# Kernel tuning notes

Hardware: AMD Instinct MI355X
Metric: run time of the kernel (lower is better)

Reference implementation:

```python
import jax, jax.numpy as jnp
import numpy as np

B, C_IN, C_OUT, N, T, KT = 8, 32, 64, 512, 24, 3
EPS = 1e-5

def leaky(x):
    return jax.nn.leaky_relu(x, 0.01)

def layer_norm(x, g, b):
    # LayerNorm over last 3 dims [C_OUT, N, T]
    m = x.mean(axis=(1, 2, 3), keepdims=True)
    v = x.var(axis=(1, 2, 3), keepdims=True)
    return (x - m) * jax.lax.rsqrt(v + EPS) * g[None] + b[None]

def conv1d_dil2(x, w):
    # Conv1d(kernel=2, dilation=2, padding=1, no bias); x: (B,C,L), w: (O,C,2)
    return jax.lax.conv_general_dilated(x, w, window_strides=(1,), padding=[(1, 1)],
                                        rhs_dilation=(2,), dimension_numbers=('NCH', 'OIH', 'NCH'))

def setup_inputs():
    key = jax.random.key(0)
    ks = jax.random.split(key, 32)
    x = jax.random.normal(ks[0], (B, C_IN, N, T), jnp.float32)
    mask = jax.random.uniform(ks[1], (N, N)) < 0.02
    adj = jnp.where(mask, jax.random.uniform(ks[2], (N, N)), 0.0).astype(jnp.float32)
    s = 0.05
    p = {
        'conv1_w': jax.random.normal(ks[3], (C_OUT, C_IN)) * s,
        'conv1_b': jnp.zeros((C_OUT,)),
        'tc_w': jax.random.normal(ks[4], (C_OUT, C_IN, 1, KT)) * s,
        'tc_b': jnp.zeros((C_OUT,)),
        'ln_g': jnp.ones((C_OUT, N, T)),
        'ln_b': jnp.zeros((C_OUT, N, T)),
        's0_ws': jax.random.normal(ks[5], (T, T)) * s,
        's0_wn': jax.random.normal(ks[6], (T, T)) * s,
        's0_b': jnp.zeros((T,)),
        's1_ws': jax.random.normal(ks[7], (T, T)) * s,
        's1_wn': jax.random.normal(ks[8], (T, T)) * s,
        's1_b': jnp.zeros((T,)),
        't_w1': jax.random.normal(ks[9], (C_OUT,)) * s,
        't_w2': jax.random.normal(ks[10], (N,)) * s,
        't_wd1': jax.random.normal(ks[11], (T, T, 2)) * s,
        't_wd2': jax.random.normal(ks[12], (C_OUT, C_OUT, 2)) * s,
        't_W': jax.random.normal(ks[13], (N, C_OUT)) * s,
        't_b': jnp.zeros((T, T)),
        't_v': jax.random.normal(ks[14], (T, T)) * s,
        'bn_g': jnp.ones((T,)),
        'bn_b': jnp.zeros((T,)),
    }
    return {'x': x, 'adj': adj, **p}

def _forward(x, adj, conv1_w, conv1_b, tc_w, tc_b, ln_g, ln_b,
             s0_ws, s0_wn, s0_b, s1_ws, s1_wn, s1_b,
             t_w1, t_w2, t_wd1, t_wd2, t_W, t_b, t_v, bn_g, bn_b):
    # 1x1 conv residual branch
    x_input = jnp.einsum('bcnl,oc->bonl', x, conv1_w) + conv1_b[None, :, None, None]
    # temporal conv (1,Kt) padding (0,1)
    x1 = jax.lax.conv_general_dilated(x, tc_w, (1, 1), [(0, 0), (1, 1)],
                                      dimension_numbers=('NCHW', 'OIHW', 'NCHW'))
    x1 = x1 + tc_b[None, :, None, None]
    x1 = leaky(layer_norm(x1, ln_g, ln_b))
    Ls = jnp.stack([jnp.eye(N, dtype=x.dtype) * 4.0, adj])          # (2,N,N)
    h = jnp.einsum('bcnl,knq->bckql', x1, Ls)                        # (B,C_OUT,2,N,T)
    M = (adj != 0).astype(x.dtype)                                   # edges u->v
    deg = jnp.maximum(M.sum(axis=0), 1.0)                            # in-degree per dst
    def sage(h, ws, wn, bias):
        neigh = jnp.einsum('bckul,uv->bckvl', h, M) / deg[None, None, None, :, None]
        return (jnp.einsum('bcknl,ml->bcknm', h, ws)
                + jnp.einsum('bcknl,ml->bcknm', neigh, wn) + bias)
    h = sage(h, s0_ws, s0_wn, s0_b)
    h = sage(h, s1_ws, s1_wn, s1_b)
    x1 = h.reshape(B, 2 * C_OUT, N, T)
    filt, gate = x1[:, :C_OUT], x1[:, C_OUT:]
    x1 = jax.nn.sigmoid(gate) * leaky(filt)                          # (B,C_OUT,N,T)
    # TATT_1
    f1 = jnp.einsum('bcnl,c->bln', x1, t_w1)                         # (B,T,N)
    f1 = conv1d_dil2(f1, t_wd1)                                      # (B,T,N)
    f2 = jnp.einsum('bcnl,n->bcl', x1, t_w2)                         # (B,C_OUT,T)
    f2 = conv1d_dil2(f2, t_wd2)                                      # (B,C_OUT,T)
    logits = jax.nn.sigmoid(jnp.einsum('bln,nc,bcq->blq', f1, t_W, f2) + t_b)
    logits = jnp.einsum('lk,bkq->blq', t_v, logits)                  # (B,T,T)
    # BatchNorm1d(T) on permuted (B,T_q,T_l), training-mode batch stats
    z = logits.transpose(0, 2, 1)
    mu = z.mean(axis=(0, 2), keepdims=True)
    var = z.var(axis=(0, 2), keepdims=True)
    z = (z - mu) * jax.lax.rsqrt(var + EPS) * bn_g[None, :, None] + bn_b[None, :, None]
    logits = z.transpose(0, 2, 1)
    A = np.zeros((T, T), np.float32); A[:12, :12] = 1.0; A[12:, 12:] = 1.0
    Bmask = jnp.asarray(-1e13 * (1.0 - A), jnp.float32)
    coefs = jax.nn.softmax(logits + Bmask, axis=-1)                  # (B,T,T)
    T_coef = coefs.transpose(0, 2, 1)
    x1 = jnp.einsum('bcnl,blq->bcnq', x1, T_coef)
    out = layer_norm(leaky(x1) + x_input, ln_g, ln_b)
    return out, adj, T_coef

def reference(x, adj, conv1_w, conv1_b, tc_w, tc_b, ln_g, ln_b,
              s0_ws, s0_wn, s0_b, s1_ws, s1_wn, s1_b,
              t_w1, t_w2, t_wd1, t_wd2, t_W, t_b, t_v, bn_g, bn_b):
    return _forward(x, adj, conv1_w, conv1_b, tc_w, tc_b, ln_g, ln_b,
                    s0_ws, s0_wn, s0_b, s1_ws, s1_wn, s1_b,
                    t_w1, t_w2, t_wd1, t_wd2, t_W, t_b, t_v, bn_g, bn_b)
```

## Files before the change

### kernel.cpp

```cpp
#include <hip/hip_runtime.h>
#include <hip/hip_bf16.h>
#include <math.h>

#define B_    8
#define CIN   32
#define CO    64
#define NN    512
#define TT    24
#define NT    (NN*TT)
#define LNCNT (CO*NT)
#define EPSL  1e-5f
#define MAXNZ 64
#define HSS   28

typedef const float* fp;
static __device__ __forceinline__ float lk(float x){ return x > 0.f ? x : 0.01f*x; }
static __device__ __forceinline__ float sg(float x){
    if(x >= 0.f){ float e = expf(-x); return 1.f/(1.f+e); }
    float e = expf(x); return e/(1.f+e);
}
static __device__ __forceinline__ unsigned pk2(float a, float b){
    __hip_bfloat16 x = __float2bfloat16(a), y = __float2bfloat16(b);
    unsigned lo = *(unsigned short*)&x, hi = *(unsigned short*)&y;
    return lo | (hi<<16);
}
static __device__ __forceinline__ float lo2f(unsigned u){ return __uint_as_float(u<<16); }
static __device__ __forceinline__ float hi2f(unsigned u){ return __uint_as_float(u & 0xffff0000u); }

__global__ __launch_bounds__(256) void k_csc(fp adj, int* cnt, int* idx, float* val){
    int e = blockIdx.x*blockDim.x + threadIdx.x;
    if(e >= NN*NN) return;
    float a = adj[e];
    if(a != 0.f){
        int u = e >> 9, q = e & 511;
        int slot = atomicAdd(&cnt[q], 1);
        if(slot < MAXNZ){ idx[q*MAXNZ+slot] = u; val[q*MAXNZ+slot] = a; }
    }
}
__global__ void k_deg(int* cnt, float* deginv){
    int q = blockIdx.x*blockDim.x + threadIdx.x;
    if(q < NN){
        int c = cnt[q];
        deginv[q] = 1.f / (c < 1 ? 1.f : (float)c);
        if(c > MAXNZ) cnt[q] = MAXNZ;
    }
}

static __device__ __forceinline__ void ldw_split(fp w, int m, int kb, uint4* hi, uint4* lo){
    float vh[8], vl[8];
    #pragma unroll
    for(int j=0;j<8;++j){
        float v = (m < TT && (kb+j) < TT) ? w[m*TT + kb + j] : 0.f;
        __hip_bfloat16 hb = __float2bfloat16(v);
        float hf = __bfloat162float(hb);
        vh[j] = hf;
        vl[j] = v - hf;
    }
    *hi = make_uint4(pk2(vh[0],vh[1]),pk2(vh[2],vh[3]),pk2(vh[4],vh[5]),pk2(vh[6],vh[7]));
    *lo = make_uint4(pk2(vl[0],vl[1]),pk2(vl[2],vl[3]),pk2(vl[4],vl[5]),pk2(vl[6],vl[7]));
}

__global__ __launch_bounds__(256) void k_wprep(fp s0ws, fp s0wn, fp s1ws, fp s1wn, uint4* wf){
    int t = threadIdx.x;
    int lane = t & 63, g = t >> 6;
    int M = g >> 1, H = g & 1;
    int m  = H*16 + (lane&15);
    int kb = (lane>>4)*8;
    for(int L=0; L<2; ++L){
        fp w = L ? (M ? s1wn : s1ws) : (M ? s0wn : s0ws);
        uint4 hi, lo;
        ldw_split(w, m, kb, &hi, &lo);
        wf[L*512 + g*128 +      lane] = hi;
        wf[L*512 + g*128 + 64 + lane] = lo;
    }
}

__global__ __launch_bounds__(256) void k_wcprep(fp w1, fp wt, uint4* wcf){
    int t = threadIdx.x;
    int lane = t & 63, g = t >> 6;
    int kb = (lane>>4)*8;
    for(int ot=0; ot<4; ++ot){
        int m = ot*16 + (lane&15);
        float vh[8], vl[8];
        #pragma unroll
        for(int j=0;j<8;++j){
            int c = kb+j;
            float v = (g==0) ? w1[m*CIN+c] : wt[(m*CIN+c)*3 + (g-1)];
            __hip_bfloat16 hb = __float2bfloat16(v);
            float hf = __bfloat162float(hb);
            vh[j]=hf; vl[j]=v-hf;
        }
        wcf[ot*512 + g*128 +      lane] = make_uint4(
            pk2(vh[0],vh[1]),pk2(vh[2],vh[3]),pk2(vh[4],vh[5]),pk2(vh[6],vh[7]));
        wcf[ot*512 + g*128 + 64 + lane] = make_uint4(
            pk2(vl[0],vl[1]),pk2(vl[2],vl[3]),pk2(vl[4],vl[5]),pk2(vl[6],vl[7]));
    }
}

typedef __attribute__((ext_vector_type(8))) short bf16x8;
typedef __attribute__((ext_vector_type(4))) float f32x4;

static __device__ __forceinline__ f32x4 MF(uint4 a, uint4 b, f32x4 c){
    union { uint4 u; bf16x8 v; } A, Bv; A.u = a; Bv.u = b;
    return __builtin_amdgcn_mfma_f32_16x16x32_bf16(A.v, Bv.v, c, 0, 0, 0);
}

#define XST 20
__global__ __launch_bounds__(256, 4) void k_conv(fp x, const uint4* wcf, fp b1, fp bt,
        float* xin, float* x1p, float* stats){
    __shared__ __attribute__((aligned(16))) unsigned xh[208*XST];
    __shared__ __attribute__((aligned(16))) unsigned xl[208*XST];
    __shared__ float red[256];
    int bid = blockIdx.x; int b = bid>>6; int n0 = (bid&63)*8;
    int tid = threadIdx.x; int lane = tid&63; int w = tid>>6;
    for(int i=tid;i<3072;i+=256){
        int cp = i/192; int r = i-cp*192; int node = r/24; int t = r-node*24;
        const float* xp = x + ((size_t)(b*CIN + 2*cp)*NN + n0+node)*TT + t;
        float a = xp[0], b2 = xp[NT];
        __hip_bfloat16 ab = __float2bfloat16(a), bb = __float2bfloat16(b2);
        float ah = __bfloat162float(ab), bh = __bfloat162float(bb);
        int row = node*26 + t + 1;
        xh[row*XST+cp] = pk2(ah, bh);
        xl[row*XST+cp] = pk2(a-ah, b2-bh);
    }
    {
        int node = tid>>5; int which = (tid>>4)&1; int j = tid&15;
        int row = node*26 + which*25;
        xh[row*XST+j]=0; xl[row*XST+j]=0;
    }
    const uint4* wb = wcf + w*512;
    uint4 h1 = wb[      lane], l1 = wb[ 64+lane];
    uint4 ht0= wb[128 + lane], lt0= wb[192+lane];
    uint4 ht1= wb[256 + lane], lt1= wb[320+lane];
    uint4 ht2= wb[384 + lane], lt2= wb[448+lane];
    int mrow = (lane>>4)*4;
    float bi0[4], bi1[4];
    #pragma unroll
    for(int r2=0;r2<4;++r2){
        int o = w*16 + mrow + r2;
        bi0[r2]=b1[o]; bi1[r2]=bt[o];
    }
    __syncthreads();
    float ls=0.f, lsq=0.f;
    int kb4 = (lane>>4)*4;
    for(int pt=0; pt<12; ++pt){
        int p = pt*16 + (lane&15);
        int node = p/24, t = p-node*24;
        int rc = (node*26 + t + 1)*XST;
        uint4 Bhm = *(const uint4*)&xh[rc - XST + kb4];
        uint4 Blm = *(const uint4*)&xl[rc - XST + kb4];
        uint4 Bhc = *(const uint4*)&xh[rc       + kb4];
        uint4 Blc = *(const uint4*)&xl[rc       + kb4];
        uint4 Bhp = *(const uint4*)&xh[rc + XST + kb4];
        uint4 Blp = *(const uint4*)&xl[rc + XST + kb4];
        f32x4 D0 = {bi0[0],bi0[1],bi0[2],bi0[3]};
        f32x4 D1 = {bi1[0],bi1[1],bi1[2],bi1[3]};
        D0 = MF(h1, Bhc, D0); D0 = MF(l1, Bhc, D0); D0 = MF(h1, Blc, D0);
        D1 = MF(ht0,Bhm, D1); D1 = MF(lt0,Bhm, D1); D1 = MF(ht0,Blm, D1);
        D1 = MF(ht1,Bhc, D1); D1 = MF(lt1,Bhc, D1); D1 = MF(ht1,Blc, D1);
        D1 = MF(ht2,Bhp, D1); D1 = MF(lt2,Bhp, D1); D1 = MF(ht2,Blp, D1);
        size_t gbase = ((size_t)(b*CO + w*16 + mrow)*NN + n0+node)*TT + t;
        #pragma unroll
        for(int r2=0;r2<4;++r2){
            xin[gbase + (size_t)r2*NT] = D0[r2];
            x1p[gbase + (size_t)r2*NT] = D1[r2];
            ls  += D1[r2];
            lsq += D1[r2]*D1[r2];
        }
    }
    red[tid]=ls; __syncthreads();
    for(int s=128;s>0;s>>=1){ if(tid<s) red[tid]+=red[tid+s]; __syncthreads(); }
    float tsum = red[0]; __syncthreads();
    red[tid]=lsq; __syncthreads();
    for(int s=128;s>0;s>>=1){ if(tid<s) red[tid]+=red[tid+s]; __syncthreads(); }
    if(tid==0){ atomicAdd(&stats[b], tsum); atomicAdd(&stats[8+b], red[0]); }
}

__global__ void k_stat(float* stats, int off){
    int b = threadIdx.x;
    if(b < 8){
        float m = stats[off+b] / (float)LNCNT;
        float v = stats[off+8+b] / (float)LNCNT - m*m;
        v = fmaxf(v, 0.f);
        stats[off+16+b] = m;
        stats[off+24+b] = rsqrtf(v + EPSL);
    }
}

__global__ __launch_bounds__(256) void k_hbuild(fp x1p, fp lng, fp lnb,
        const float* stats, const int* cnt, const int* idx, const float* val, unsigned* h){
    __shared__ float xs[NN*HSS];
    int blk = blockIdx.x; int b = blk >> 6; int c = blk & 63;
    int tid = threadIdx.x;
    float m = stats[16+b], inv = stats[24+b];
    fp src = x1p + (size_t)(b*CO + c)*NT;
    for(int i=tid;i<NT;i+=256){
        int n = i/TT, t = i%TT;
        xs[n*HSS + t] = lk((src[i] - m)*inv*lng[c*NT + i] + lnb[c*NT + i]);
    }
    __syncthreads();
    unsigned* h0 = h + (size_t)((b*CO+c)*2 + 0)*(NT/2);
    unsigned* h1 = h0 + NT/2;
    #pragma unroll
    for(int half=0; half<2; ++half){
        int n = tid + half*256;
        float t1[TT], acc[TT];
        const float4* sp = (const float4*)&xs[n*HSS];
        #pragma unroll
        for(int k=0;k<6;++k){
            float4 v = sp[k];
            t1[4*k]=v.x; t1[4*k+1]=v.y; t1[4*k+2]=v.z; t1[4*k+3]=v.w;
        }
        #pragma unroll
        for(int l=0;l<TT;++l) acc[l]=0.f;
        int cq = cnt[n];
        for(int j=0;j<cq;++j){
            int u = idx[n*MAXNZ+j];
            float v = val[n*MAXNZ+j];
            const float4* rp = (const float4*)&xs[u*HSS];
            #pragma unroll
            for(int k=0;k<6;++k){
                float4 w = rp[k];
                acc[4*k]+=v*w.x; acc[4*k+1]+=v*w.y; acc[4*k+2]+=v*w.z; acc[4*k+3]+=v*w.w;
            }
        }
        #pragma unroll
        for(int k=0;k<3;++k){
            *(uint4*)(h0 + n*12 + 4*k) = make_uint4(
                pk2(4.f*t1[8*k],  4.f*t1[8*k+1]), pk2(4.f*t1[8*k+2],4.f*t1[8*k+3]),
                pk2(4.f*t1[8*k+4],4.f*t1[8*k+5]), pk2(4.f*t1[8*k+6],4.f*t1[8*k+7]));
            *(uint4*)(h1 + n*12 + 4*k) = make_uint4(
                pk2(acc[8*k],  acc[8*k+1]), pk2(acc[8*k+2],acc[8*k+3]),
                pk2(acc[8*k+4],acc[8*k+5]), pk2(acc[8*k+6],acc[8*k+7]));
        }
    }
}

static __device__ __forceinline__ void acc8(float* t, uint4 q){
    t[0]+=lo2f(q.x); t[1]+=hi2f(q.x); t[2]+=lo2f(q.y); t[3]+=hi2f(q.y);
    t[4]+=lo2f(q.z); t[5]+=hi2f(q.z); t[6]+=lo2f(q.w); t[7]+=hi2f(q.w);
}

#define GBODY(u) { int ro=(u)*12; \
    uint4 q0=*(const uint4*)&hsb[ro]; \
    uint4 q1=*(const uint4*)&hsb[ro+4]; \
    uint4 q2=*(const uint4*)&hsb[ro+8]; \
    acc8(t2,q0); acc8(t2+8,q1); acc8(t2+16,q2); }
#define GSTEP(J,U) if((J)<cq) GBODY(U)

__global__ __launch_bounds__(512, 4) void k_sageF(unsigned* h, const uint4* wf,
        fp s0b, fp s1b, const int* cnt, const int* idx, const float* deginv){
    __shared__ unsigned hsb[NN*12];
    int tid  = threadIdx.x;
    int lane = tid & 63;
    int wv   = tid >> 6;
    unsigned* base = h + (size_t)blockIdx.x*(NT/2);

    for(int i=tid;i<1536;i+=512) ((uint4*)hsb)[i] = ((const uint4*)base)[i];
    int n  = tid;
    int cq = cnt[n];
    float di = deginv[n];
    int4 i0 = *(const int4*)&idx[n*MAXNZ+0];
    int4 i1 = *(const int4*)&idx[n*MAXNZ+4];
    int4 i2 = *(const int4*)&idx[n*MAXNZ+8];
    __syncthreads();

    for(int layer=0; layer<2; ++layer){
        const uint4* wl = wf + layer*512;
        uint4 wsHiA = wl[      lane], wsLoA = wl[ 64+lane];
        uint4 wsHiB = wl[128 + lane], wsLoB = wl[192+lane];
        uint4 wnHiA = wl[256 + lane], wnLoA = wl[320+lane];
        uint4 wnHiB = wl[384 + lane], wnLoB = wl[448+lane];
        fp Bp = layer ? s1b : s0b;
        float biA[4], biB[4];
        #pragma unroll
        for(int r=0;r<4;++r){
            biA[r] = Bp[(lane>>4)*4 + r];
            int m2 = 16 + (lane>>4)*4 + r;
            biB[r] = (m2 < TT) ? Bp[m2] : 0.f;
        }

        float t2[TT];
        #pragma unroll
        for(int l=0;l<TT;++l) t2[l]=0.f;
        GSTEP(0,i0.x) GSTEP(1,i0.y) GSTEP(2,i0.z) GSTEP(3,i0.w)
        GSTEP(4,i1.x) GSTEP(5,i1.y) GSTEP(6,i1.z) GSTEP(7,i1.w)
        GSTEP(8,i2.x) GSTEP(9,i2.y) GSTEP(10,i2.z) GSTEP(11,i2.w)
        for(int j=12;j<cq;++j){ int u=idx[n*MAXNZ+j]; GBODY(u) }
        #pragma unroll
        for(int l=0;l<TT;++l) t2[l]*=di;

        uint4 b0[4];
        #pragma unroll
        for(int i=0;i<4;++i) b0[i]=make_uint4(0,0,0,0);
        if(lane < 48){
            #pragma unroll
            for(int i=0;i<4;++i){
                int nn_ = wv*64 + i*16 + (lane&15);
                b0[i] = *(const uint4*)&hsb[nn_*12 + ((lane>>4)<<2)];
            }
        }
        __syncthreads();

        *(uint4*)&hsb[n*12  ] = make_uint4(
            pk2(t2[0],t2[1]),  pk2(t2[2],t2[3]),  pk2(t2[4],t2[5]),  pk2(t2[6],t2[7]));
        *(uint4*)&hsb[n*12+4] = make_uint4(
            pk2(t2[8],t2[9]),  pk2(t2[10],t2[11]),pk2(t2[12],t2[13]),pk2(t2[14],t2[15]));
        *(uint4*)&hsb[n*12+8] = make_uint4(
            pk2(t2[16],t2[17]),pk2(t2[18],t2[19]),pk2(t2[20],t2[21]),pk2(t2[22],t2[23]));
        __syncthreads();

        uint4 b1[4];
        #pragma unroll
        for(int i=0;i<4;++i) b1[i]=make_uint4(0,0,0,0);
        if(lane < 48){
            #pragma unroll
            for(int i=0;i<4;++i){
                int nn_ = wv*64 + i*16 + (lane&15);
                b1[i] = *(const uint4*)&hsb[nn_*12 + ((lane>>4)<<2)];
            }
        }
        f32x4 Da[4], Db[4];
        #pragma unroll
        for(int i=0;i<4;++i){
            Da[i] = (f32x4){biA[0],biA[1],biA[2],biA[3]};
            Db[i] = (f32x4){biB[0],biB[1],biB[2],biB[3]};
            Da[i] = MF(wsHiA, b0[i], Da[i]);
            Da[i] = MF(wsLoA, b0[i], Da[i]);
            Da[i] = MF(wnHiA, b1[i], Da[i]);
            Da[i] = MF(wnLoA, b1[i], Da[i]);
            Db[i] = MF(wsHiB, b0[i], Db[i]);
            Db[i] = MF(wsLoB, b0[i], Db[i]);
            Db[i] = MF(wnHiB, b1[i], Db[i]);
            Db[i] = MF(wnLoB, b1[i], Db[i]);
        }
        __syncthreads();
        #pragma unroll
        for(int i=0;i<4;++i){
            int nn_ = wv*64 + i*16 + (lane&15);
            int o = (lane>>4)*2;
            *(uint2*)&hsb[nn_*12 + o] =
                make_uint2(pk2(Da[i][0],Da[i][1]), pk2(Da[i][2],Da[i][3]));
            if(lane < 32){
                *(uint2*)&hsb[nn_*12 + 8 + (lane>>4)*2] =
                    make_uint2(pk2(Db[i][0],Db[i][1]), pk2(Db[i][2],Db[i][3]));
            }
        }
        __syncthreads();
    }
    for(int i=tid;i<1536;i+=512) ((uint4*)base)[i] = ((const uint4*)hsb)[i];
}

__global__ __launch_bounds__(192) void k_f1(const unsigned* h, fp w1, float* f1){
    int blk = blockIdx.x; int b = blk>>6; int n0 = (blk&63)*8;
    int tid = threadIdx.x;
    float acc = 0.f;
    const unsigned* fb = h + (size_t)b*CO*NT + n0*12;
    const unsigned* gb = fb + (size_t)CO*(NT/2);
    int e = tid;
    for(int c=0;c<CO;++c){
        float w = w1[c];
        unsigned f = fb[(size_t)c*(NT/2) + (e>>1)];
        unsigned g = gb[(size_t)c*(NT/2) + (e>>1)];
        float fv = (e&1) ? hi2f(f) : lo2f(f);
        float gv = (e&1) ? hi2f(g) : lo2f(g);
        acc += sg(gv)*lk(fv)*w;
    }
    int nl = e/TT, t = e%TT;
    f1[(b*TT+t)*NN + n0+nl] = acc;
}

__global__ __launch_bounds__(256) void k_f2(const unsigned* h, fp w2, float* f2){
    __shared__ float red[256*TT];
    int blk = blockIdx.x; int b = blk/CO; int c = blk%CO;
    int tid = threadIdx.x;
    float acc[TT];
    #pragma unroll
    for(int l=0;l<TT;++l) acc[l]=0.f;
    const unsigned* fb = h + (size_t)b*CO*NT + (size_t)c*(NT/2);
    const unsigned* gb = fb + (size_t)CO*(NT/2);
    for(int n=tid;n<NN;n+=256){
        float w = w2[n];
        #pragma unroll
        for(int k=0;k<3;++k){
            uint4 f = *(const uint4*)(fb + n*12 + 4*k);
            uint4 g = *(const uint4*)(gb + n*12 + 4*k);
            acc[8*k  ] += sg(lo2f(g.x))*lk(lo2f(f.x))*w;
            acc[8*k+1] += sg(hi2f(g.x))*lk(hi2f(f.x))*w;
            acc[8*k+2] += sg(lo2f(g.y))*lk(lo2f(f.y))*w;
            acc[8*k+3] += sg(hi2f(g.y))*lk(hi2f(f.y))*w;
            acc[8*k+4] += sg(lo2f(g.z))*lk(lo2f(f.z))*w;
            acc[8*k+5] += sg(hi2f(g.z))*lk(hi2f(f.z))*w;
            acc[8*k+6] += sg(lo2f(g.w))*lk(lo2f(f.w))*w;
            acc[8*k+7] += sg(hi2f(g.w))*lk(hi2f(f.w))*w;
        }
    }
    #pragma unroll
    for(int l=0;l<TT;++l) red[tid*TT+l]=acc[l];
    __syncthreads();
    for(int s=128;s>0;s>>=1){
        if(tid<s){
            #pragma unroll
            for(int l=0;l<TT;++l) red[tid*TT+l]+=red[(tid+s)*TT+l];
        }
        __syncthreads();
    }
    if(tid<TT) f2[(b*CO+c)*TT+tid] = red[tid];
}

__global__ __launch_bounds__(256) void k_conv_f1(fp f1, fp wd1, float* f1c){
    __shared__ float fs[TT][130];
    __shared__ float w0[TT*TT], w1a[TT*TT];
    int bid = blockIdx.x; int b = bid>>2; int n0 = (bid&3)*128;
    int tid=threadIdx.x;
    for(int i=tid;i<TT*130;i+=256){
        int l=i/130, col=i%130; int n = n0+col-1;
        fs[l][col] = (n>=0 && n<NN) ? f1[(b*TT+l)*NN+n] : 0.f;
    }
    for(int i=tid;i<TT*TT;i+=256){ w0[i]=wd1[i*2]; w1a[i]=wd1[i*2+1]; }
    __syncthreads();
    for(int j=tid;j<TT*128;j+=256){
        int o=j>>7, nn=j&127;
        float acc=0.f;
        #pragma unroll
        for(int i=0;i<TT;++i) acc += fs[i][nn]*w0[o*TT+i] + fs[i][nn+2]*w1a[o*TT+i];
        f1c[(b*TT+o)*NN+n0+nn]=acc;
    }
}

__global__ __launch_bounds__(256) void k_conv_f2(fp f2, fp wd2, float* f2c){
    __shared__ float fs[CO][TT+2];
    __shared__ float w0[CO*CO], w1a[CO*CO];
    int b = blockIdx.x; int tid=threadIdx.x;
    for(int i=tid;i<CO*TT;i+=256){ int c=i/TT,l=i%TT; fs[c][l+1]=f2[(b*CO+c)*TT+l]; }
    for(int c=tid;c<CO;c+=256){ fs[c][0]=0.f; fs[c][TT+1]=0.f; }
    for(int i=tid;i<CO*CO;i+=256){ w0[i]=wd2[i*2]; w1a[i]=wd2[i*2+1]; }
    __syncthreads();
    for(int j=tid;j<CO*TT;j+=256){
        int o=j/TT, l=j%TT;
        float acc=0.f;
        for(int i=0;i<CO;++i) acc += fs[i][l]*w0[o*CO+i] + fs[i][l+2]*w1a[o*CO+i];
        f2c[(b*CO+o)*TT+l]=acc;
    }
}

__global__ __launch_bounds__(384) void k_g1(fp f1c, fp tW, float* g1){
    __shared__ float fs[6*NN];
    int blk=blockIdx.x; int b=blk>>2; int part=blk&3;
    int tid=threadIdx.x;
    for(int i=tid;i<6*NN;i+=384) fs[i]=f1c[b*TT*NN + part*6*NN + i];
    __syncthreads();
    int c = tid & 63; int r = tid >> 6;
    float acc=0.f;
    for(int n=0;n<NN;++n) acc += fs[r*NN + n]*tW[n*CO + c];
    g1[(b*TT + part*6 + r)*CO + c] = acc;
}

__global__ __launch_bounds__(1024) void k_logits(fp g1, fp f2c,
        fp tbias, fp tv, fp bng, fp bnb, float* coefs, float* tco){
    __shared__ float sig[B_*TT*TT];
    __shared__ float lg2[B_*TT*TT];
    __shared__ float muq[TT], scq[TT], shq[TT];
    int tid=threadIdx.x;
    for(int j=tid;j<B_*TT*TT;j+=1024){
        int b=j/(TT*TT); int r=j%(TT*TT); int l=r/TT; int q=r%TT;
        float acc = tbias[l*TT+q];
        fp gg = g1 + (b*TT+l)*CO;
        fp ff = f2c + b*CO*TT + q;
        for(int c=0;c<CO;++c) acc += gg[c]*ff[c*TT];
        sig[j] = sg(acc);
    }
    __syncthreads();
    for(int j=tid;j<B_*TT*TT;j+=1024){
        int b=j/(TT*TT); int r=j%(TT*TT); int l=r/TT; int q=r%TT;
        float acc=0.f;
        for(int k=0;k<TT;++k) acc += tv[l*TT+k]*sig[(b*TT+k)*TT+q];
        lg2[j]=acc;
    }
    __syncthreads();
    if(tid<TT){
        int q=tid;
        float s=0.f;
        for(int b=0;b<B_;++b) for(int l=0;l<TT;++l) s += lg2[(b*TT+l)*TT+q];
        float mu = s/192.f;
        float v=0.f;
        for(int b=0;b<B_;++b) for(int l=0;l<TT;++l){ float d = lg2[(b*TT+l)*TT+q]-mu; v += d*d; }
        v = fmaxf(v/192.f, 0.f);
        muq[q]=mu; scq[q]=rsqrtf(v+EPSL)*bng[q]; shq[q]=bnb[q];
    }
    __syncthreads();
    if(tid<192){
        int b=tid/TT, l=tid%TT;
        int base = (l<12)?0:12;
        float z[12];
        float mx=-1e30f;
        #pragma unroll
        for(int r=0;r<12;++r){
            int q=base+r;
            float zv=(lg2[(b*TT+l)*TT+q]-muq[q])*scq[q]+shq[q];
            z[r]=zv; mx = fmaxf(mx,zv);
        }
        float s=0.f;
        #pragma unroll
        for(int r=0;r<12;++r){ z[r]=expf(z[r]-mx); s+=z[r]; }
        float is=1.f/s;
        for(int q=0;q<TT;++q){
            float cf = (q>=base && q<base+12) ? z[q-base]*is : 0.f;
            coefs[(b*TT+l)*TT+q]=cf;
            tco[(b*TT+q)*TT+l]=cf;
        }
    }
}

__global__ __launch_bounds__(256, 4) void k_apply(const unsigned* h, fp xin, fp coefs,
        float* y, float* stats){
    __shared__ float cf[TT*TT];
    __shared__ float red[256];
    int blk=blockIdx.x; int b=blk>>7; int c=(blk>>1)&63; int half=blk&1;
    int tid=threadIdx.x;
    for(int i=tid;i<TT*TT;i+=256) cf[i]=coefs[b*TT*TT+i];
    __syncthreads();
    int n = half*256 + tid;
    const unsigned* fb = h + (size_t)b*CO*NT + (size_t)c*(NT/2) + n*12;
    const unsigned* gb = fb + (size_t)CO*(NT/2);
    fp xrow = xin + (size_t)(b*CO+c)*NT + n*TT;
    float* yrow = y + (size_t)(b*CO+c)*NT + n*TT;
    float row[TT];
    #pragma unroll
    for(int k=0;k<3;++k){
        uint4 f = *(const uint4*)(fb + 4*k);
        uint4 g = *(const uint4*)(gb + 4*k);
        row[8*k  ] = sg(lo2f(g.x))*lk(lo2f(f.x));
        row[8*k+1] = sg(hi2f(g.x))*lk(hi2f(f.x));
        row[8*k+2] = sg(lo2f(g.y))*lk(lo2f(f.y));
        row[8*k+3] = sg(hi2f(g.y))*lk(hi2f(f.y));
        row[8*k+4] = sg(lo2f(g.z))*lk(lo2f(f.z));
        row[8*k+5] = sg(hi2f(g.z))*lk(hi2f(f.z));
        row[8*k+6] = sg(lo2f(g.w))*lk(lo2f(f.w));
        row[8*k+7] = sg(hi2f(g.w))*lk(hi2f(f.w));
    }
    float ls=0.f, lsq=0.f;
    #pragma unroll
    for(int k=0;k<6;++k){
        float4 u = *(const float4*)(xrow + 4*k);
        float a0=0.f, a1=0.f, a2=0.f, a3=0.f;
        #pragma unroll
        for(int l=0;l<TT;++l){
            float r = row[l];
            a0 += r*cf[(4*k  )*TT+l];
            a1 += r*cf[(4*k+1)*TT+l];
            a2 += r*cf[(4*k+2)*TT+l];
            a3 += r*cf[(4*k+3)*TT+l];
        }
        float y0 = lk(a0)+u.x, y1 = lk(a1)+u.y, y2 = lk(a2)+u.z, y3 = lk(a3)+u.w;
        *(float4*)(yrow + 4*k) = make_float4(y0,y1,y2,y3);
        ls  += y0+y1+y2+y3;
        lsq += y0*y0+y1*y1+y2*y2+y3*y3;
    }
    red[tid]=ls; __syncthreads();
    for(int s=128;s>0;s>>=1){ if(tid<s) red[tid]+=red[tid+s]; __syncthreads(); }
    float t0=red[0]; __syncthreads();
    red[tid]=lsq; __syncthreads();
    for(int s=128;s>0;s>>=1){ if(tid<s) red[tid]+=red[tid+s]; __syncthreads(); }
    if(tid==0){ atomicAdd(&stats[32+b], t0); atomicAdd(&stats[40+b], red[0]); }
}

__global__ void k_final(fp y, fp lng, fp lnb, const float* stats, float* out){
    int tot = B_*CO*NT;
    for(int i = blockIdx.x*blockDim.x + threadIdx.x; i<tot; i+=gridDim.x*blockDim.x){
        int b = i/LNCNT; int r = i%LNCNT;
        out[i] = (y[i]-stats[48+b])*stats[56+b]*lng[r]+lnb[r];
    }
}

extern "C" void kernel_launch(void* const* d_in, const int* in_sizes, int n_in,
                              void* d_out, int out_size, void* d_ws, size_t ws_size,
                              hipStream_t stream){
    fp x    = (fp)d_in[0];
    fp adj  = (fp)d_in[1];
    fp w1   = (fp)d_in[2];
    fp b1   = (fp)d_in[3];
    fp wt   = (fp)d_in[4];
    fp bt   = (fp)d_in[5];
    fp lng  = (fp)d_in[6];
    fp lnb  = (fp)d_in[7];
    fp s0ws = (fp)d_in[8];
    fp s0wn = (fp)d_in[9];
    fp s0b  = (fp)d_in[10];
    fp s1ws = (fp)d_in[11];
    fp s1wn = (fp)d_in[12];
    fp s1b  = (fp)d_in[13];
    fp tw1  = (fp)d_in[14];
    fp tw2  = (fp)d_in[15];
    fp twd1 = (fp)d_in[16];
    fp twd2 = (fp)d_in[17];
    fp tW   = (fp)d_in[18];
    fp tbias= (fp)d_in[19];
    fp tv   = (fp)d_in[20];
    fp bng  = (fp)d_in[21];
    fp bnb  = (fp)d_in[22];

    float* W = (float*)d_ws;
    int*   CNTp = (int*)(W+256);
    float* DEG  = W+768;
    int*   IDXp = (int*)(W+1280);
    float* VALp = W+34048;
    float* F1   = W+66816;
    float* F1C  = W+165120;
    float* F2   = W+263424;
    float* F2C  = W+275712;
    float* G1   = W+288000;
    float* CF   = W+300288;
    float* XIN  = W+304896;
    float* X1   = W+6596352;
    uint4* WFq  = (uint4*)(W+12887808);
    uint4* WCF  = (uint4*)(W+12891904);
    unsigned* HA = (unsigned*)(W+19179264);
    float* Y    = W+31762176;

    float* oout   = (float*)d_out;
    float* o_adj  = oout + 6291456;
    float* o_tc   = oout + 6291456 + 262144;

    hipMemsetAsync(W, 0, 768*sizeof(float), stream);
    k_csc<<<1024,256,0,stream>>>(adj, CNTp, IDXp, VALp);
    k_deg<<<2,256,0,stream>>>(CNTp, DEG);
    k_wprep<<<1,256,0,stream>>>(s0ws, s0wn, s1ws, s1wn, WFq);
    k_wcprep<<<1,256,0,stream>>>(w1, wt, WCF);
    k_conv<<<512,256,0,stream>>>(x, WCF, b1, bt, XIN, X1, W);
    k_stat<<<1,64,0,stream>>>(W, 0);
    k_hbuild<<<512,256,0,stream>>>(X1, lng, lnb, W, CNTp, IDXp, VALp, HA);
    k_sageF<<<1024,512,0,stream>>>(HA, WFq, s0b, s1b, CNTp, IDXp, DEG);
    k_f1<<<512,192,0,stream>>>(HA, tw1, F1);
    k_f2<<<512,256,0,stream>>>(HA, tw2, F2);
    k_conv_f1<<<32,256,0,stream>>>(F1, twd1, F1C);
    k_conv_f2<<<8,256,0,stream>>>(F2, twd2, F2C);
    k_g1<<<32,384,0,stream>>>(F1C, tW, G1);
    k_logits<<<1,1024,0,stream>>>(G1, F2C, tbias, tv, bng, bnb, CF, o_tc);
    hipMemcpyAsync(o_adj, d_in[1], 262144*sizeof(float), hipMemcpyDeviceToDevice, stream);
    k_apply<<<1024,256,0,stream>>>(HA, XIN, CF, Y, W);
    k_stat<<<1,64,0,stream>>>(W, 32);
    k_final<<<2048,256,0,stream>>>(Y, lng, lnb, W, oout);
}
```

Measured before the change: 396.6 us.

## Widen hbuild to one thread per node, vectorize loads, pack sage accumulators

k_hbuild now runs 512 threads so each thread handles one node. It loads the normalization inputs as float4 and prefetches the first twelve neighbor indices and values before an unrolled gather. k_sageF accumulates into float2 vectors to encourage packed FP32 adds, and packs MFMA outputs to bf16 right away to cut live registers. k_f2 pads its reduction array stride to 25 to avoid LDS bank conflicts. These touch several unrelated kernels and risk register pressure under the new launch bounds.

```diff
diff --git a/kernel.cpp b/kernel.cpp
--- a/kernel.cpp
+++ b/kernel.cpp
@@ -99,6 +99,7 @@
 
 typedef __attribute__((ext_vector_type(8))) short bf16x8;
 typedef __attribute__((ext_vector_type(4))) float f32x4;
+typedef __attribute__((ext_vector_type(2))) float f32x2;
 
 static __device__ __forceinline__ f32x4 MF(uint4 a, uint4 b, f32x4 c){
     union { uint4 u; bf16x8 v; } A, Bv; A.u = a; Bv.u = b;
@@ -187,65 +188,82 @@
     }
 }
 
-__global__ __launch_bounds__(256) void k_hbuild(fp x1p, fp lng, fp lnb,
+__global__ __launch_bounds__(512, 4) void k_hbuild(fp x1p, fp lng, fp lnb,
         const float* stats, const int* cnt, const int* idx, const float* val, unsigned* h){
     __shared__ float xs[NN*HSS];
     int blk = blockIdx.x; int b = blk >> 6; int c = blk & 63;
     int tid = threadIdx.x;
     float m = stats[16+b], inv = stats[24+b];
-    fp src = x1p + (size_t)(b*CO + c)*NT;
-    for(int i=tid;i<NT;i+=256){
-        int n = i/TT, t = i%TT;
-        xs[n*HSS + t] = lk((src[i] - m)*inv*lng[c*NT + i] + lnb[c*NT + i]);
-    }
-    __syncthreads();
-    unsigned* h0 = h + (size_t)((b*CO+c)*2 + 0)*(NT/2);
+    fp src  = x1p + (size_t)(b*CO + c)*NT;
+    fp gsrc = lng + (size_t)c*NT;
+    fp bsrc = lnb + (size_t)c*NT;
+    for(int i4=tid;i4<NT/4;i4+=512){
+        int i = i4*4;
+        int n = i/TT, t = i-n*TT;
+        float4 s  = *(const float4*)(src + i);
+        float4 g  = *(const float4*)(gsrc + i);
+        float4 bb = *(const float4*)(bsrc + i);
+        *(float4*)&xs[n*HSS + t] = make_float4(
+            lk((s.x-m)*inv*g.x+bb.x), lk((s.y-m)*inv*g.y+bb.y),
+            lk((s.z-m)*inv*g.z+bb.z), lk((s.w-m)*inv*g.w+bb.w));
+    }
+    int n = tid;
+    int cq = cnt[n];
+    int4 j0 = *(const int4*)&idx[n*MAXNZ+0];
+    int4 j1 = *(const int4*)&idx[n*MAXNZ+4];
+    int4 j2 = *(const int4*)&idx[n*MAXNZ+8];
+    float4 v0 = *(const float4*)&val[n*MAXNZ+0];
+    float4 v1 = *(const float4*)&val[n*MAXNZ+4];
+    float4 v2 = *(const float4*)&val[n*MAXNZ+8];
+    __syncthreads();
+    float acc[TT];
+    #pragma unroll
+    for(int l=0;l<TT;++l) acc[l]=0.f;
+#define HB(J,U,V) if((J)<cq){ const float4* rp=(const float4*)&xs[(U)*HSS]; \
+    _Pragma("unroll") for(int k=0;k<6;++k){ float4 wv=rp[k]; \
+        acc[4*k]+=(V)*wv.x; acc[4*k+1]+=(V)*wv.y; acc[4*k+2]+=(V)*wv.z; acc[4*k+3]+=(V)*wv.w; } }
+    HB(0,j0.x,v0.x) HB(1,j0.y,v0.y) HB(2,j0.z,v0.z) HB(3,j0.w,v0.w)
+    HB(4,j1.x,v1.x) HB(5,j1.y,v1.y) HB(6,j1.z,v1.z) HB(7,j1.w,v1.w)
+    HB(8,j2.x,v2.x) HB(9,j2.y,v2.y) HB(10,j2.z,v2.z) HB(11,j2.w,v2.w)
+    for(int j=12;j<cq;++j){
+        int u = idx[n*MAXNZ+j]; float v = val[n*MAXNZ+j];
+        const float4* rp = (const float4*)&xs[u*HSS];
+        #pragma unroll
+        for(int k=0;k<6;++k){ float4 wv=rp[k];
+            acc[4*k]+=v*wv.x; acc[4*k+1]+=v*wv.y; acc[4*k+2]+=v*wv.z; acc[4*k+3]+=v*wv.w; }
+    }
+    float t1[TT];
+    const float4* sp = (const float4*)&xs[n*HSS];
+    #pragma unroll
+    for(int k=0;k<6;++k){
+        float4 v = sp[k];
+        t1[4*k]=v.x; t1[4*k+1]=v.y; t1[4*k+2]=v.z; t1[4*k+3]=v.w;
+    }
+    unsigned* h0 = h + (size_t)((b*CO+c)*2)*(NT/2);
     unsigned* h1 = h0 + NT/2;
     #pragma unroll
-    for(int half=0; half<2; ++half){
-        int n = tid + half*256;
-        float t1[TT], acc[TT];
-        const float4* sp = (const float4*)&xs[n*HSS];
-        #pragma unroll
-        for(int k=0;k<6;++k){
-            float4 v = sp[k];
-            t1[4*k]=v.x; t1[4*k+1]=v.y; t1[4*k+2]=v.z; t1[4*k+3]=v.w;
-        }
-        #pragma unroll
-        for(int l=0;l<TT;++l) acc[l]=0.f;
-        int cq = cnt[n];
-        for(int j=0;j<cq;++j){
-            int u = idx[n*MAXNZ+j];
-            float v = val[n*MAXNZ+j];
-            const float4* rp = (const float4*)&xs[u*HSS];
-            #pragma unroll
-            for(int k=0;k<6;++k){
-                float4 w = rp[k];
-                acc[4*k]+=v*w.x; acc[4*k+1]+=v*w.y; acc[4*k+2]+=v*w.z; acc[4*k+3]+=v*w.w;
-            }
-        }
-        #pragma unroll
-        for(int k=0;k<3;++k){
-            *(uint4*)(h0 + n*12 + 4*k) = make_uint4(
-                pk2(4.f*t1[8*k],  4.f*t1[8*k+1]), pk2(4.f*t1[8*k+2],4.f*t1[8*k+3]),
-                pk2(4.f*t1[8*k+4],4.f*t1[8*k+5]), pk2(4.f*t1[8*k+6],4.f*t1[8*k+7]));
-            *(uint4*)(h1 + n*12 + 4*k) = make_uint4(
-                pk2(acc[8*k],  acc[8*k+1]), pk2(acc[8*k+2],acc[8*k+3]),
-                pk2(acc[8*k+4],acc[8*k+5]), pk2(acc[8*k+6],acc[8*k+7]));
-        }
-    }
-}
-
-static __device__ __forceinline__ void acc8(float* t, uint4 q){
-    t[0]+=lo2f(q.x); t[1]+=hi2f(q.x); t[2]+=lo2f(q.y); t[3]+=hi2f(q.y);
-    t[4]+=lo2f(q.z); t[5]+=hi2f(q.z); t[6]+=lo2f(q.w); t[7]+=hi2f(q.w);
+    for(int k=0;k<3;++k){
+        *(uint4*)(h0 + n*12 + 4*k) = make_uint4(
+            pk2(4.f*t1[8*k],  4.f*t1[8*k+1]), pk2(4.f*t1[8*k+2],4.f*t1[8*k+3]),
+            pk2(4.f*t1[8*k+4],4.f*t1[8*k+5]), pk2(4.f*t1[8*k+6],4.f*t1[8*k+7]));
+        *(uint4*)(h1 + n*12 + 4*k) = make_uint4(
+            pk2(acc[8*k],  acc[8*k+1]), pk2(acc[8*k+2],acc[8*k+3]),
+            pk2(acc[8*k+4],acc[8*k+5]), pk2(acc[8*k+6],acc[8*k+7]));
+    }
+}
+
+static __device__ __forceinline__ void acc8v(f32x2* t, uint4 q){
+    t[0] += (f32x2){lo2f(q.x), hi2f(q.x)};
+    t[1] += (f32x2){lo2f(q.y), hi2f(q.y)};
+    t[2] += (f32x2){lo2f(q.z), hi2f(q.z)};
+    t[3] += (f32x2){lo2f(q.w), hi2f(q.w)};
 }
 
 #define GBODY(u) { int ro=(u)*12; \
     uint4 q0=*(const uint4*)&hsb[ro]; \
     uint4 q1=*(const uint4*)&hsb[ro+4]; \
     uint4 q2=*(const uint4*)&hsb[ro+8]; \
-    acc8(t2,q0); acc8(t2+8,q1); acc8(t2+16,q2); }
+    acc8v(t2v,q0); acc8v(t2v+4,q1); acc8v(t2v+8,q2); }
 #define GSTEP(J,U) if((J)<cq) GBODY(U)
 
 __global__ __launch_bounds__(512, 4) void k_sageF(unsigned* h, const uint4* wf,
@@ -280,15 +298,15 @@
             biB[r] = (m2 < TT) ? Bp[m2] : 0.f;
         }
 
-        float t2[TT];
-        #pragma unroll
-        for(int l=0;l<TT;++l) t2[l]=0.f;
+        f32x2 t2v[12];
+        #pragma unroll
+        for(int l=0;l<12;++l) t2v[l] = (f32x2){0.f,0.f};
         GSTEP(0,i0.x) GSTEP(1,i0.y) GSTEP(2,i0.z) GSTEP(3,i0.w)
         GSTEP(4,i1.x) GSTEP(5,i1.y) GSTEP(6,i1.z) GSTEP(7,i1.w)
         GSTEP(8,i2.x) GSTEP(9,i2.y) GSTEP(10,i2.z) GSTEP(11,i2.w)
         for(int j=12;j<cq;++j){ int u=idx[n*MAXNZ+j]; GBODY(u) }
         #pragma unroll
-        for(int l=0;l<TT;++l) t2[l]*=di;
+        for(int l=0;l<12;++l) t2v[l] *= di;
 
         uint4 b0[4];
         #pragma unroll
@@ -303,11 +321,14 @@
         __syncthreads();
 
         *(uint4*)&hsb[n*12  ] = make_uint4(
-            pk2(t2[0],t2[1]),  pk2(t2[2],t2[3]),  pk2(t2[4],t2[5]),  pk2(t2[6],t2[7]));
+            pk2(t2v[0].x,t2v[0].y), pk2(t2v[1].x,t2v[1].y),
+            pk2(t2v[2].x,t2v[2].y), pk2(t2v[3].x,t2v[3].y));
         *(uint4*)&hsb[n*12+4] = make_uint4(
-            pk2(t2[8],t2[9]),  pk2(t2[10],t2[11]),pk2(t2[12],t2[13]),pk2(t2[14],t2[15]));
+            pk2(t2v[4].x,t2v[4].y), pk2(t2v[5].x,t2v[5].y),
+            pk2(t2v[6].x,t2v[6].y), pk2(t2v[7].x,t2v[7].y));
         *(uint4*)&hsb[n*12+8] = make_uint4(
-            pk2(t2[16],t2[17]),pk2(t2[18],t2[19]),pk2(t2[20],t2[21]),pk2(t2[22],t2[23]));
+            pk2(t2v[8].x,t2v[8].y), pk2(t2v[9].x,t2v[9].y),
+            pk2(t2v[10].x,t2v[10].y), pk2(t2v[11].x,t2v[11].y));
         __syncthreads();
 
         uint4 b1[4];
@@ -320,30 +341,30 @@
                 b1[i] = *(const uint4*)&hsb[nn_*12 + ((lane>>4)<<2)];
             }
         }
-        f32x4 Da[4], Db[4];
+        uint2 pa[4], pb[4];
         #pragma unroll
         for(int i=0;i<4;++i){
-            Da[i] = (f32x4){biA[0],biA[1],biA[2],biA[3]};
-            Db[i] = (f32x4){biB[0],biB[1],biB[2],biB[3]};
-            Da[i] = MF(wsHiA, b0[i], Da[i]);
-            Da[i] = MF(wsLoA, b0[i], Da[i]);
-            Da[i] = MF(wnHiA, b1[i], Da[i]);
-            Da[i] = MF(wnLoA, b1[i], Da[i]);
-            Db[i] = MF(wsHiB, b0[i], Db[i]);
-            Db[i] = MF(wsLoB, b0[i], Db[i]);
-            Db[i] = MF(wnHiB, b1[i], Db[i]);
-            Db[i] = MF(wnLoB, b1[i], Db[i]);
+            f32x4 Da = {biA[0],biA[1],biA[2],biA[3]};
+            f32x4 Db = {biB[0],biB[1],biB[2],biB[3]};
+            Da = MF(wsHiA, b0[i], Da);
+            Da = MF(wsLoA, b0[i], Da);
+            Da = MF(wnHiA, b1[i], Da);
+            Da = MF(wnLoA, b1[i], Da);
+            Db = MF(wsHiB, b0[i], Db);
+            Db = MF(wsLoB, b0[i], Db);
+            Db = MF(wnHiB, b1[i], Db);
+            Db = MF(wnLoB, b1[i], Db);
+            pa[i] = make_uint2(pk2(Da[0],Da[1]), pk2(Da[2],Da[3]));
+            pb[i] = make_uint2(pk2(Db[0],Db[1]), pk2(Db[2],Db[3]));
         }
         __syncthreads();
         #pragma unroll
         for(int i=0;i<4;++i){
             int nn_ = wv*64 + i*16 + (lane&15);
             int o = (lane>>4)*2;
-            *(uint2*)&hsb[nn_*12 + o] =
-                make_uint2(pk2(Da[i][0],Da[i][1]), pk2(Da[i][2],Da[i][3]));
+            *(uint2*)&hsb[nn_*12 + o] = pa[i];
             if(lane < 32){
-                *(uint2*)&hsb[nn_*12 + 8 + (lane>>4)*2] =
-                    make_uint2(pk2(Db[i][0],Db[i][1]), pk2(Db[i][2],Db[i][3]));
+                *(uint2*)&hsb[nn_*12 + 8 + (lane>>4)*2] = pb[i];
             }
         }
         __syncthreads();
@@ -370,8 +391,9 @@
     f1[(b*TT+t)*NN + n0+nl] = acc;
 }
 
+#define F2S 25
 __global__ __launch_bounds__(256) void k_f2(const unsigned* h, fp w2, float* f2){
-    __shared__ float red[256*TT];
+    __shared__ float red[256*F2S];
     int blk = blockIdx.x; int b = blk/CO; int c = blk%CO;
     int tid = threadIdx.x;
     float acc[TT];
@@ -396,12 +418,12 @@
         }
     }
     #pragma unroll
-    for(int l=0;l<TT;++l) red[tid*TT+l]=acc[l];
+    for(int l=0;l<TT;++l) red[tid*F2S+l]=acc[l];
     __syncthreads();
     for(int s=128;s>0;s>>=1){
         if(tid<s){
             #pragma unroll
-            for(int l=0;l<TT;++l) red[tid*TT+l]+=red[(tid+s)*TT+l];
+            for(int l=0;l<TT;++l) red[tid*F2S+l]+=red[(tid+s)*F2S+l];
         }
         __syncthreads();
     }
@@ -629,7 +651,7 @@
     k_wcprep<<<1,256,0,stream>>>(w1, wt, WCF);
     k_conv<<<512,256,0,stream>>>(x, WCF, b1, bt, XIN, X1, W);
     k_stat<<<1,64,0,stream>>>(W, 0);
-    k_hbuild<<<512,256,0,stream>>>(X1, lng, lnb, W, CNTp, IDXp, VALp, HA);
+    k_hbuild<<<512,512,0,stream>>>(X1, lng, lnb, W, CNTp, IDXp, VALp, HA);
     k_sageF<<<1024,512,0,stream>>>(HA, WFq, s0b, s1b, CNTp, IDXp, DEG);
     k_f1<<<512,192,0,stream>>>(HA, tw1, F1);
     k_f2<<<512,256,0,stream>>>(HA, tw2, F2);
```

Measured after the change: 393.7 us. About the same (-0.7%).
